# Kernel optimization log

Hardware: AMD Instinct MI355X
Metric: run time of the kernel (lower is better)

The kernel has to match this reference:

```python
import jax, jax.numpy as jnp
import numpy as np

EMBED = 2048
HEADS = 16
GROUPS = 4
HEAD_DIM = EMBED // HEADS  # 128
REPEATS = HEADS // GROUPS  # 4


def setup_inputs() -> dict:
    key = jax.random.key(0)
    ks = jax.random.split(key, 9)
    s = 1.0 / np.sqrt(EMBED)
    kv_dim = GROUPS * HEAD_DIM
    return {
        "x": jax.random.normal(ks[0], (2, 2048, EMBED), dtype=jnp.float32),
        "Wq": jax.random.normal(ks[1], (EMBED, EMBED), dtype=jnp.float32) * s,
        "bq": jnp.zeros((EMBED,), dtype=jnp.float32),
        "Wk": jax.random.normal(ks[2], (EMBED, kv_dim), dtype=jnp.float32) * s,
        "bk": jnp.zeros((kv_dim,), dtype=jnp.float32),
        "Wv": jax.random.normal(ks[3], (EMBED, kv_dim), dtype=jnp.float32) * s,
        "bv": jnp.zeros((kv_dim,), dtype=jnp.float32),
        "Wo": jax.random.normal(ks[4], (EMBED, EMBED), dtype=jnp.float32) * s,
        "bo": jnp.zeros((EMBED,), dtype=jnp.float32),
    }


def reference(x, Wq, bq, Wk, bk, Wv, bv, Wo, bo):
    b, t, e = x.shape
    q = x @ Wq + bq                                   # [b,t,e]
    k = x @ Wk + bk                                   # [b,t,g*d]
    v = x @ Wv + bv
    # [b, g, r, t, d] for q; [b, g, t, d] for k,v (repeat_interleave == group-major)
    q = q.reshape(b, t, GROUPS, REPEATS, HEAD_DIM).transpose(0, 2, 3, 1, 4)
    k = k.reshape(b, t, GROUPS, HEAD_DIM).transpose(0, 2, 1, 3)
    v = v.reshape(b, t, GROUPS, HEAD_DIM).transpose(0, 2, 1, 3)
    scale = 1.0 / np.sqrt(HEAD_DIM)
    scores = jnp.einsum('bgrqd,bgkd->bgrqk', q, k) * scale
    causal = jnp.tril(jnp.ones((t, t), dtype=bool))
    scores = jnp.where(causal, scores, -jnp.inf)
    w = jax.nn.softmax(scores, axis=-1)
    out = jnp.einsum('bgrqk,bgkd->bgrqd', w, v)       # [b,g,r,t,d]
    out = out.transpose(0, 3, 1, 2, 4).reshape(b, t, e)
    return out @ Wo + bo
```

## Files before the change

### kernel.cpp

```cpp
#include <hip/hip_runtime.h>
#include <cstdint>

typedef __bf16 bf16;
typedef __attribute__((ext_vector_type(8))) __bf16 bf16x8;
typedef __attribute__((ext_vector_type(4))) __bf16 bf16x4;
typedef __attribute__((ext_vector_type(4))) float f32x4;

__device__ __forceinline__ void load_lds16(const void* g, void* l) {
  __builtin_amdgcn_global_load_lds(
      (const __attribute__((address_space(1))) unsigned int*)g,
      (__attribute__((address_space(3))) unsigned int*)l, 16, 0, 0);
}

__device__ __forceinline__ float fast_exp2(float x) {
  float r;
  asm volatile("v_exp_f32 %0, %1" : "=v"(r) : "v"(x));
  return r;
}

template <bool OUT_F32>
__global__ __launch_bounds__(256) void gemm_bt(
    const bf16* __restrict__ A, const bf16* __restrict__ Bt,
    const float* __restrict__ bias, void* __restrict__ Cv,
    int M, int N, int K) {
  __shared__ __align__(16) bf16 sA[128 * 64];
  __shared__ __align__(16) bf16 sB[128 * 64];
  const int t = threadIdx.x;
  const int w = t >> 6, lane = t & 63;
  const int quad = lane >> 4, l16 = lane & 15;
  const int wm = (w >> 1) * 64, wn = (w & 1) * 64;
  const int bm = blockIdx.y * 128, bn = blockIdx.x * 128;

  f32x4 acc[4][4] = {};
  const int srow = lane >> 3;
  const int sg = lane & 7;

  for (int kt = 0; kt < (K >> 6); ++kt) {
    const int k0 = kt << 6;
#pragma unroll
    for (int c2 = 0; c2 < 4; ++c2) {
      int c = c2 * 4 + w;
      int row = c * 8 + srow;
      int gg = sg ^ (row & 7);
      load_lds16(A + (int64_t)(bm + row) * K + k0 + gg * 8, sA + c * 512);
      load_lds16(Bt + (int64_t)(bn + row) * K + k0 + gg * 8, sB + c * 512);
    }
    asm volatile("s_waitcnt vmcnt(0)" ::: "memory");
    __syncthreads();
#pragma unroll
    for (int ks = 0; ks < 2; ++ks) {
      bf16x8 af[4], bfr[4];
#pragma unroll
      for (int i = 0; i < 4; ++i) {
        int m = wm + i * 16 + l16;
        af[i] = *(const bf16x8*)(sA + m * 64 + (((ks * 4 + quad) ^ (l16 & 7)) * 8));
        int n = wn + i * 16 + l16;
        bfr[i] = *(const bf16x8*)(sB + n * 64 + (((ks * 4 + quad) ^ (l16 & 7)) * 8));
      }
#pragma unroll
      for (int i = 0; i < 4; ++i)
#pragma unroll
        for (int j = 0; j < 4; ++j)
          acc[i][j] = __builtin_amdgcn_mfma_f32_16x16x32_bf16(af[i], bfr[j],
                                                              acc[i][j], 0, 0, 0);
    }
    __syncthreads();
  }
#pragma unroll
  for (int i = 0; i < 4; ++i) {
    int gm = bm + wm + i * 16 + quad * 4;
#pragma unroll
    for (int j = 0; j < 4; ++j) {
      int gn = bn + wn + j * 16 + l16;
      float bvv = bias ? bias[gn] : 0.0f;
#pragma unroll
      for (int r = 0; r < 4; ++r) {
        float v = acc[i][j][r] + bvv;
        if (OUT_F32)
          ((float*)Cv)[(int64_t)(gm + r) * N + gn] = v;
        else
          ((bf16*)Cv)[(int64_t)(gm + r) * N + gn] = (bf16)v;
      }
    }
  }
}

__global__ __launch_bounds__(256, 2) void attn(
    const bf16* __restrict__ QKV, const bf16* __restrict__ Vt,
    bf16* __restrict__ Out) {
  constexpr float CC = 0.08838834764831845f * 1.44269504088896f;
  __shared__ __align__(16) bf16 sK[2][64 * 128];
  __shared__ __align__(16) bf16 sV[2][128 * 64];
  __shared__ __align__(16) bf16 sP[128 * 64];

  const int t = threadIdx.x;
  const int w = t >> 6, lane = t & 63;
  const int quad = lane >> 4, l16 = lane & 15;
  const int p = blockIdx.x, h = blockIdx.y, b = blockIdx.z;
  const int g = h >> 2;
  const int wr0 = w * 16;
  const int kbase = 2048 + g * 128;
  const bf16* vtb = Vt + (int64_t)((b * 4 + g) * 128) * 2048;
  const int rk = lane >> 4, rv = lane >> 3, sgv = lane & 7;
  const int qrow0A = p * 64, qrow0B = (31 - p) * 64;
  const int niters = 32 - p;

  bf16x8 qreg[2][4];
#pragma unroll
  for (int u = 0; u < 2; ++u) {
    int qr = (u == 0 ? qrow0A : qrow0B);
#pragma unroll
    for (int ks = 0; ks < 4; ++ks)
      qreg[u][ks] = *(const bf16x8*)(QKV +
          (int64_t)(b * 2048 + qr + wr0 + l16) * 3072 + h * 128 + ks * 32 +
          quad * 8);
  }

  f32x4 oacc[2][8] = {};
  float mrow[2] = {-3.0e38f, -3.0e38f};
  float lrow[2] = {0.f, 0.f};

  auto stage = [&](int n0, bf16* sKb, bf16* sVb) {
#pragma unroll
    for (int c2 = 0; c2 < 4; ++c2) {
      int c = c2 * 4 + w;
      int rowk = c * 4 + rk;
      int ggk = (l16 & 8) | ((l16 ^ rowk) & 7);
      load_lds16(QKV + (int64_t)(b * 2048 + n0 + rowk) * 3072 + kbase + ggk * 8,
                 sKb + c * 512);
      int rowv = c * 8 + rv;
      int ggv = sgv ^ (rowv & 7);
      load_lds16(vtb + (int64_t)rowv * 2048 + n0 + ggv * 8, sVb + c * 512);
    }
  };

  stage(0, sK[0], sV[0]);

  const int prowA = wr0 + l16;
  const int prowB = 64 + wr0 + l16;

  for (int it = 0; it < niters; ++it) {
    const int cur = it & 1;
    const int n0 = it * 64;
    bf16* sKc = sK[cur];
    bf16* sVc = sV[cur];
    const bool actA = (it <= p);

    asm volatile("s_waitcnt vmcnt(0)\n\ts_barrier" ::: "memory");
    if (it + 1 < niters) stage(n0 + 64, sK[cur ^ 1], sV[cur ^ 1]);

    f32x4 sacc[2][4] = {};
    if (actA) {
#pragma unroll
      for (int ks = 0; ks < 4; ++ks) {
        bf16x8 ak[4];
#pragma unroll
        for (int mj = 0; mj < 4; ++mj) {
          int kvr = mj * 16 + l16;
          int G = ks * 4 + quad;
          int slot = (G & 8) | ((G ^ kvr) & 7);
          ak[mj] = *(const bf16x8*)(sKc + kvr * 128 + slot * 8);
        }
#pragma unroll
        for (int mj = 0; mj < 4; ++mj) {
          sacc[0][mj] = __builtin_amdgcn_mfma_f32_16x16x32_bf16(
              ak[mj], qreg[0][ks], sacc[0][mj], 0, 0, 0);
          sacc[1][mj] = __builtin_amdgcn_mfma_f32_16x16x32_bf16(
              ak[mj], qreg[1][ks], sacc[1][mj], 0, 0, 0);
        }
      }
    } else {
#pragma unroll
      for (int ks = 0; ks < 4; ++ks) {
        bf16x8 ak[4];
#pragma unroll
        for (int mj = 0; mj < 4; ++mj) {
          int kvr = mj * 16 + l16;
          int G = ks * 4 + quad;
          int slot = (G & 8) | ((G ^ kvr) & 7);
          ak[mj] = *(const bf16x8*)(sKc + kvr * 128 + slot * 8);
        }
#pragma unroll
        for (int mj = 0; mj < 4; ++mj)
          sacc[1][mj] = __builtin_amdgcn_mfma_f32_16x16x32_bf16(
              ak[mj], qreg[1][ks], sacc[1][mj], 0, 0, 0);
      }
    }

    auto softmax_u = [&](int u, bool last, int qrow0u, int prow) {
      if (last) {
        int q = qrow0u + wr0 + l16;
#pragma unroll
        for (int mj = 0; mj < 4; ++mj)
#pragma unroll
          for (int r = 0; r < 4; ++r) {
            int kv = n0 + mj * 16 + quad * 4 + r;
            if (kv > q) sacc[u][mj][r] = -3.0e38f;
          }
      }
      f32x4 m01, m23;
#pragma unroll
      for (int r = 0; r < 4; ++r) {
        m01[r] = fmaxf(sacc[u][0][r], sacc[u][1][r]);
        m23[r] = fmaxf(sacc[u][2][r], sacc[u][3][r]);
      }
      float mx = fmaxf(fmaxf(fmaxf(m01[0], m01[1]), fmaxf(m01[2], m01[3])),
                       fmaxf(fmaxf(m23[0], m23[1]), fmaxf(m23[2], m23[3])));
      mx = fmaxf(mx, __shfl_xor(mx, 16));
      mx = fmaxf(mx, __shfl_xor(mx, 32));
      float mnew = fmaxf(mrow[u], mx);
      float alpha = fast_exp2((mrow[u] - mnew) * CC);
      float rs = 0.f;
#pragma unroll
      for (int mj = 0; mj < 4; ++mj) {
        bf16x4 p4;
#pragma unroll
        for (int r = 0; r < 4; ++r) {
          float pv = fast_exp2((sacc[u][mj][r] - mnew) * CC);
          rs += pv;
          p4[r] = (bf16)pv;
        }
        int g16 = mj * 2 + (quad >> 1);
        int off = prow * 64 + ((g16 ^ (prow & 7)) * 8) + (quad & 1) * 4;
        *(bf16x4*)(sP + off) = p4;
      }
      rs += __shfl_xor(rs, 16);
      rs += __shfl_xor(rs, 32);
      lrow[u] = lrow[u] * alpha + rs;
      mrow[u] = mnew;
#pragma unroll
      for (int dj = 0; dj < 8; ++dj)
#pragma unroll
        for (int r = 0; r < 4; ++r) oacc[u][dj][r] *= alpha;
    };
    if (actA) softmax_u(0, it == p, qrow0A, prowA);
    softmax_u(1, it == niters - 1, qrow0B, prowB);

    asm volatile("s_waitcnt lgkmcnt(0)" ::: "memory");

#pragma unroll
    for (int ks2 = 0; ks2 < 2; ++ks2) {
      int G = ks2 * 4 + quad;
      bf16x8 bpA, bpB;
      if (actA)
        bpA = *(const bf16x8*)(sP + prowA * 64 + ((G ^ (prowA & 7)) * 8));
      bpB = *(const bf16x8*)(sP + prowB * 64 + ((G ^ (prowB & 7)) * 8));
      bf16x8 av[8];
#pragma unroll
      for (int dj = 0; dj < 8; ++dj) {
        int d = dj * 16 + l16;
        av[dj] = *(const bf16x8*)(sVc + d * 64 + ((G ^ (d & 7)) * 8));
      }
      if (actA) {
#pragma unroll
        for (int dj = 0; dj < 8; ++dj) {
          oacc[0][dj] = __builtin_amdgcn_mfma_f32_16x16x32_bf16(
              av[dj], bpA, oacc[0][dj], 0, 0, 0);
          oacc[1][dj] = __builtin_amdgcn_mfma_f32_16x16x32_bf16(
              av[dj], bpB, oacc[1][dj], 0, 0, 0);
        }
      } else {
#pragma unroll
        for (int dj = 0; dj < 8; ++dj)
          oacc[1][dj] = __builtin_amdgcn_mfma_f32_16x16x32_bf16(
              av[dj], bpB, oacc[1][dj], 0, 0, 0);
      }
    }
  }

#pragma unroll
  for (int u = 0; u < 2; ++u) {
    int qrow0u = (u == 0 ? qrow0A : qrow0B);
    float inv = 1.0f / lrow[u];
    int64_t grow = b * 2048 + qrow0u + wr0 + l16;
#pragma unroll
    for (int dj = 0; dj < 8; ++dj) {
      bf16x4 o4;
#pragma unroll
      for (int r = 0; r < 4; ++r) o4[r] = (bf16)(oacc[u][dj][r] * inv);
      *(bf16x4*)(Out + grow * 2048 + h * 128 + dj * 16 + quad * 4) = o4;
    }
  }
}

__global__ void convert_x(const float* __restrict__ x, bf16* __restrict__ xb) {
  int idx = blockIdx.x * 256 + threadIdx.x;
  float4 v = ((const float4*)x)[idx];
  bf16x4 o = {(bf16)v.x, (bf16)v.y, (bf16)v.z, (bf16)v.w};
  ((bf16x4*)xb)[idx] = o;
}

__global__ void transpose_w(const float* __restrict__ W, bf16* __restrict__ Wt,
                            int K, int N) {
  __shared__ float tile[32][33];
  int bx = blockIdx.x, by = blockIdx.y;
  int tx = threadIdx.x, ty = threadIdx.y;
#pragma unroll
  for (int q2 = 0; q2 < 4; ++q2)
    tile[ty + q2 * 8][tx] = W[(int64_t)(by * 32 + ty + q2 * 8) * N + bx * 32 + tx];
  __syncthreads();
#pragma unroll
  for (int q2 = 0; q2 < 4; ++q2)
    Wt[(int64_t)(bx * 32 + ty + q2 * 8) * K + by * 32 + tx] =
        (bf16)tile[tx][ty + q2 * 8];
}

__global__ void transpose_v(const bf16* __restrict__ QKV, bf16* __restrict__ Vt) {
  __shared__ bf16 tile[32][34];
  int dt = blockIdx.x, tt = blockIdx.y, bg = blockIdx.z;
  int b = bg >> 2, g = bg & 3;
  int tx = threadIdx.x, ty = threadIdx.y;
#pragma unroll
  for (int q2 = 0; q2 < 4; ++q2) {
    int trow = tt * 32 + ty + q2 * 8;
    tile[ty + q2 * 8][tx] =
        QKV[(int64_t)(b * 2048 + trow) * 3072 + 2560 + g * 128 + dt * 32 + tx];
  }
  __syncthreads();
#pragma unroll
  for (int q2 = 0; q2 < 4; ++q2) {
    int d = dt * 32 + ty + q2 * 8;
    Vt[(int64_t)(bg * 128 + d) * 2048 + tt * 32 + tx] = tile[tx][ty + q2 * 8];
  }
}

__global__ void concat_bias(const float* __restrict__ bq,
                            const float* __restrict__ bk,
                            const float* __restrict__ bv,
                            float* __restrict__ o) {
  int i = blockIdx.x * 256 + threadIdx.x;
  if (i < 3072)
    o[i] = i < 2048 ? bq[i] : (i < 2560 ? bk[i - 2048] : bv[i - 2560]);
}

extern "C" void kernel_launch(void* const* d_in, const int* in_sizes, int n_in,
                              void* d_out, int out_size, void* d_ws,
                              size_t ws_size, hipStream_t stream) {
  const float* x = (const float*)d_in[0];
  const float* Wq = (const float*)d_in[1];
  const float* bq = (const float*)d_in[2];
  const float* Wk = (const float*)d_in[3];
  const float* bk = (const float*)d_in[4];
  const float* Wv = (const float*)d_in[5];
  const float* bv = (const float*)d_in[6];
  const float* Wo = (const float*)d_in[7];
  const float* bo = (const float*)d_in[8];
  float* out = (float*)d_out;

  char* ws = (char*)d_ws;
  bf16* xb = (bf16*)(ws);
  bf16* wqkvT = (bf16*)(ws + 16777216);
  bf16* woT = (bf16*)(ws + 29360128);
  float* bqkv = (float*)(ws + 37748736);
  bf16* qkv = (bf16*)(ws + 37761024);
  bf16* vt = (bf16*)(ws + 62926848);
  bf16* attnb = (bf16*)(ws + 67121152);

  convert_x<<<8192, 256, 0, stream>>>(x, xb);
  dim3 tb(32, 8);
  transpose_w<<<dim3(64, 64), tb, 0, stream>>>(Wq, wqkvT, 2048, 2048);
  transpose_w<<<dim3(16, 64), tb, 0, stream>>>(Wk, wqkvT + 2048 * 2048, 2048, 512);
  transpose_w<<<dim3(16, 64), tb, 0, stream>>>(Wv, wqkvT + 2560 * 2048, 2048, 512);
  transpose_w<<<dim3(64, 64), tb, 0, stream>>>(Wo, woT, 2048, 2048);
  concat_bias<<<12, 256, 0, stream>>>(bq, bk, bv, bqkv);

  gemm_bt<false><<<dim3(24, 32), 256, 0, stream>>>(xb, wqkvT, bqkv, qkv, 4096,
                                                   3072, 2048);
  transpose_v<<<dim3(4, 64, 8), tb, 0, stream>>>(qkv, vt);
  attn<<<dim3(16, 16, 2), 256, 0, stream>>>(qkv, vt, attnb);
  gemm_bt<true><<<dim3(16, 32), 256, 0, stream>>>(attnb, woT, bo, out, 4096,
                                                  2048, 2048);
}
```

Baseline: 319.1 us.

## Split attention KV range across two blocks with combine kernel, smaller KV tiles

Attention work per query-pair block is split along the KV dimension into two halves (z index), doubling the grid, with each half writing unnormalized outputs plus row max/sum to workspace. A new combine kernel then merges the two partial softmax results. KV tiles shrink from 64 to 32 rows to cut LDS use, and occupancy is raised to 3 blocks per CU. The weight-transpose kernel also moves to 64x64 tiles. The aim is better load balance and occupancy in attention, at the cost of an extra kernel, extra global traffic for the partial outputs, and reuse of workspace regions.

Result: slower. 368.5 us (+15.5%).

```diff
diff --git a/kernel.cpp b/kernel.cpp
--- a/kernel.cpp
+++ b/kernel.cpp
@@ -85,25 +85,32 @@
   }
 }
 
-__global__ __launch_bounds__(256, 2) void attn(
+__global__ __launch_bounds__(256, 3) void attn(
     const bf16* __restrict__ QKV, const bf16* __restrict__ Vt,
-    bf16* __restrict__ Out) {
+    bf16* __restrict__ O1, bf16* __restrict__ O2,
+    float* __restrict__ m_arr, float* __restrict__ l_arr) {
   constexpr float CC = 0.08838834764831845f * 1.44269504088896f;
-  __shared__ __align__(16) bf16 sK[2][64 * 128];
-  __shared__ __align__(16) bf16 sV[2][128 * 64];
-  __shared__ __align__(16) bf16 sP[128 * 64];
+  __shared__ __align__(16) bf16 sK[2][32 * 128];
+  __shared__ __align__(16) bf16 sV[2][128 * 32];
+  __shared__ __align__(16) bf16 sP[128 * 32];
 
   const int t = threadIdx.x;
   const int w = t >> 6, lane = t & 63;
   const int quad = lane >> 4, l16 = lane & 15;
-  const int p = blockIdx.x, h = blockIdx.y, b = blockIdx.z;
+  const int p = blockIdx.x, h = blockIdx.y;
+  const int b = blockIdx.z >> 1, z = blockIdx.z & 1;
   const int g = h >> 2;
   const int wr0 = w * 16;
   const int kbase = 2048 + g * 128;
   const bf16* vtb = Vt + (int64_t)((b * 4 + g) * 128) * 2048;
-  const int rk = lane >> 4, rv = lane >> 3, sgv = lane & 7;
   const int qrow0A = p * 64, qrow0B = (31 - p) * 64;
-  const int niters = 32 - p;
+  const int NV = (z == 0) ? (32 - p) : 33;
+
+  auto map = [&](int vi, int& tl, bool& aA, bool& aB) {
+    if (z == 0) { tl = vi; aA = (vi <= p); aB = true; }
+    else if (vi <= p) { tl = p + 1 + vi; aA = true; aB = false; }
+    else { tl = 31 - 2 * p + vi; aA = false; aB = true; }
+  };
 
   bf16x8 qreg[2][4];
 #pragma unroll
@@ -120,99 +127,93 @@
   float mrow[2] = {-3.0e38f, -3.0e38f};
   float lrow[2] = {0.f, 0.f};
 
-  auto stage = [&](int n0, bf16* sKb, bf16* sVb) {
-#pragma unroll
-    for (int c2 = 0; c2 < 4; ++c2) {
-      int c = c2 * 4 + w;
+  const int rk = lane >> 4;
+  const int rv = lane >> 2, gv = lane & 3;
+
+  auto stage = [&](int tl, int buf) {
+    int n0 = tl * 32;
+#pragma unroll
+    for (int r = 0; r < 2; ++r) {
+      int c = r * 4 + w;
       int rowk = c * 4 + rk;
       int ggk = (l16 & 8) | ((l16 ^ rowk) & 7);
       load_lds16(QKV + (int64_t)(b * 2048 + n0 + rowk) * 3072 + kbase + ggk * 8,
-                 sKb + c * 512);
-      int rowv = c * 8 + rv;
-      int ggv = sgv ^ (rowv & 7);
-      load_lds16(vtb + (int64_t)rowv * 2048 + n0 + ggv * 8, sVb + c * 512);
+                 sK[buf] + c * 512);
+      int rowv = c * 16 + rv;
+      int ggv = gv ^ (rowv & 3);
+      load_lds16(vtb + (int64_t)rowv * 2048 + n0 + ggv * 8, sV[buf] + c * 512);
     }
   };
 
-  stage(0, sK[0], sV[0]);
+  {
+    int tl0; bool a0, b0;
+    map(0, tl0, a0, b0);
+    stage(tl0, 0);
+  }
 
   const int prowA = wr0 + l16;
   const int prowB = 64 + wr0 + l16;
 
-  for (int it = 0; it < niters; ++it) {
-    const int cur = it & 1;
-    const int n0 = it * 64;
+  for (int vi = 0; vi < NV; ++vi) {
+    const int cur = vi & 1;
+    int tl; bool actA, actB;
+    map(vi, tl, actA, actB);
+    const int n0 = tl * 32;
     bf16* sKc = sK[cur];
     bf16* sVc = sV[cur];
-    const bool actA = (it <= p);
 
     asm volatile("s_waitcnt vmcnt(0)\n\ts_barrier" ::: "memory");
-    if (it + 1 < niters) stage(n0 + 64, sK[cur ^ 1], sV[cur ^ 1]);
-
-    f32x4 sacc[2][4] = {};
-    if (actA) {
-#pragma unroll
-      for (int ks = 0; ks < 4; ++ks) {
-        bf16x8 ak[4];
-#pragma unroll
-        for (int mj = 0; mj < 4; ++mj) {
-          int kvr = mj * 16 + l16;
-          int G = ks * 4 + quad;
-          int slot = (G & 8) | ((G ^ kvr) & 7);
-          ak[mj] = *(const bf16x8*)(sKc + kvr * 128 + slot * 8);
-        }
-#pragma unroll
-        for (int mj = 0; mj < 4; ++mj) {
+    if (vi + 1 < NV) {
+      int tln; bool an, bn_;
+      map(vi + 1, tln, an, bn_);
+      stage(tln, cur ^ 1);
+    }
+
+    f32x4 sacc[2][2] = {};
+#pragma unroll
+    for (int ks = 0; ks < 4; ++ks) {
+      bf16x8 ak[2];
+#pragma unroll
+      for (int mj = 0; mj < 2; ++mj) {
+        int kvr = mj * 16 + l16;
+        int G = ks * 4 + quad;
+        int slot = (G & 8) | ((G ^ kvr) & 7);
+        ak[mj] = *(const bf16x8*)(sKc + kvr * 128 + slot * 8);
+      }
+      if (actA)
+#pragma unroll
+        for (int mj = 0; mj < 2; ++mj)
           sacc[0][mj] = __builtin_amdgcn_mfma_f32_16x16x32_bf16(
               ak[mj], qreg[0][ks], sacc[0][mj], 0, 0, 0);
+      if (actB)
+#pragma unroll
+        for (int mj = 0; mj < 2; ++mj)
           sacc[1][mj] = __builtin_amdgcn_mfma_f32_16x16x32_bf16(
               ak[mj], qreg[1][ks], sacc[1][mj], 0, 0, 0);
-        }
-      }
-    } else {
-#pragma unroll
-      for (int ks = 0; ks < 4; ++ks) {
-        bf16x8 ak[4];
-#pragma unroll
-        for (int mj = 0; mj < 4; ++mj) {
-          int kvr = mj * 16 + l16;
-          int G = ks * 4 + quad;
-          int slot = (G & 8) | ((G ^ kvr) & 7);
-          ak[mj] = *(const bf16x8*)(sKc + kvr * 128 + slot * 8);
-        }
-#pragma unroll
-        for (int mj = 0; mj < 4; ++mj)
-          sacc[1][mj] = __builtin_amdgcn_mfma_f32_16x16x32_bf16(
-              ak[mj], qreg[1][ks], sacc[1][mj], 0, 0, 0);
-      }
-    }
-
-    auto softmax_u = [&](int u, bool last, int qrow0u, int prow) {
-      if (last) {
+    }
+
+    auto softmax_u = [&](int u, int qrow0u, int prow) {
+      if (n0 + 31 > qrow0u + wr0) {
         int q = qrow0u + wr0 + l16;
 #pragma unroll
-        for (int mj = 0; mj < 4; ++mj)
+        for (int mj = 0; mj < 2; ++mj)
 #pragma unroll
           for (int r = 0; r < 4; ++r) {
             int kv = n0 + mj * 16 + quad * 4 + r;
             if (kv > q) sacc[u][mj][r] = -3.0e38f;
           }
       }
-      f32x4 m01, m23;
-#pragma unroll
-      for (int r = 0; r < 4; ++r) {
-        m01[r] = fmaxf(sacc[u][0][r], sacc[u][1][r]);
-        m23[r] = fmaxf(sacc[u][2][r], sacc[u][3][r]);
-      }
-      float mx = fmaxf(fmaxf(fmaxf(m01[0], m01[1]), fmaxf(m01[2], m01[3])),
-                       fmaxf(fmaxf(m23[0], m23[1]), fmaxf(m23[2], m23[3])));
+      f32x4 m01;
+#pragma unroll
+      for (int r = 0; r < 4; ++r) m01[r] = fmaxf(sacc[u][0][r], sacc[u][1][r]);
+      float mx = fmaxf(fmaxf(m01[0], m01[1]), fmaxf(m01[2], m01[3]));
       mx = fmaxf(mx, __shfl_xor(mx, 16));
       mx = fmaxf(mx, __shfl_xor(mx, 32));
       float mnew = fmaxf(mrow[u], mx);
       float alpha = fast_exp2((mrow[u] - mnew) * CC);
       float rs = 0.f;
 #pragma unroll
-      for (int mj = 0; mj < 4; ++mj) {
+      for (int mj = 0; mj < 2; ++mj) {
         bf16x4 p4;
 #pragma unroll
         for (int r = 0; r < 4; ++r) {
@@ -221,7 +222,7 @@
           p4[r] = (bf16)pv;
         }
         int g16 = mj * 2 + (quad >> 1);
-        int off = prow * 64 + ((g16 ^ (prow & 7)) * 8) + (quad & 1) * 4;
+        int off = prow * 32 + ((g16 ^ (prow & 3)) * 8) + (quad & 1) * 4;
         *(bf16x4*)(sP + off) = p4;
       }
       rs += __shfl_xor(rs, 16);
@@ -233,54 +234,73 @@
 #pragma unroll
         for (int r = 0; r < 4; ++r) oacc[u][dj][r] *= alpha;
     };
-    if (actA) softmax_u(0, it == p, qrow0A, prowA);
-    softmax_u(1, it == niters - 1, qrow0B, prowB);
+    if (actA) softmax_u(0, qrow0A, prowA);
+    if (actB) softmax_u(1, qrow0B, prowB);
 
     asm volatile("s_waitcnt lgkmcnt(0)" ::: "memory");
 
-#pragma unroll
-    for (int ks2 = 0; ks2 < 2; ++ks2) {
-      int G = ks2 * 4 + quad;
-      bf16x8 bpA, bpB;
+    bf16x8 bpA, bpB;
+    if (actA) bpA = *(const bf16x8*)(sP + prowA * 32 + ((quad ^ (prowA & 3)) * 8));
+    if (actB) bpB = *(const bf16x8*)(sP + prowB * 32 + ((quad ^ (prowB & 3)) * 8));
+#pragma unroll
+    for (int dj = 0; dj < 8; ++dj) {
+      int d = dj * 16 + l16;
+      bf16x8 av = *(const bf16x8*)(sVc + d * 32 + ((quad ^ (d & 3)) * 8));
       if (actA)
-        bpA = *(const bf16x8*)(sP + prowA * 64 + ((G ^ (prowA & 7)) * 8));
-      bpB = *(const bf16x8*)(sP + prowB * 64 + ((G ^ (prowB & 7)) * 8));
-      bf16x8 av[8];
-#pragma unroll
-      for (int dj = 0; dj < 8; ++dj) {
-        int d = dj * 16 + l16;
-        av[dj] = *(const bf16x8*)(sVc + d * 64 + ((G ^ (d & 7)) * 8));
-      }
-      if (actA) {
-#pragma unroll
-        for (int dj = 0; dj < 8; ++dj) {
-          oacc[0][dj] = __builtin_amdgcn_mfma_f32_16x16x32_bf16(
-              av[dj], bpA, oacc[0][dj], 0, 0, 0);
-          oacc[1][dj] = __builtin_amdgcn_mfma_f32_16x16x32_bf16(
-              av[dj], bpB, oacc[1][dj], 0, 0, 0);
-        }
-      } else {
-#pragma unroll
-        for (int dj = 0; dj < 8; ++dj)
-          oacc[1][dj] = __builtin_amdgcn_mfma_f32_16x16x32_bf16(
-              av[dj], bpB, oacc[1][dj], 0, 0, 0);
-      }
-    }
-  }
-
+        oacc[0][dj] = __builtin_amdgcn_mfma_f32_16x16x32_bf16(av, bpA,
+                                                             oacc[0][dj], 0, 0, 0);
+      if (actB)
+        oacc[1][dj] = __builtin_amdgcn_mfma_f32_16x16x32_bf16(av, bpB,
+                                                             oacc[1][dj], 0, 0, 0);
+    }
+  }
+
+  bf16* OutP = (z == 0) ? O1 : O2;
 #pragma unroll
   for (int u = 0; u < 2; ++u) {
     int qrow0u = (u == 0 ? qrow0A : qrow0B);
-    float inv = 1.0f / lrow[u];
     int64_t grow = b * 2048 + qrow0u + wr0 + l16;
 #pragma unroll
     for (int dj = 0; dj < 8; ++dj) {
       bf16x4 o4;
 #pragma unroll
-      for (int r = 0; r < 4; ++r) o4[r] = (bf16)(oacc[u][dj][r] * inv);
-      *(bf16x4*)(Out + grow * 2048 + h * 128 + dj * 16 + quad * 4) = o4;
-    }
-  }
+      for (int r = 0; r < 4; ++r) o4[r] = (bf16)oacc[u][dj][r];
+      *(bf16x4*)(OutP + grow * 2048 + h * 128 + dj * 16 + quad * 4) = o4;
+    }
+    if (quad == 0) {
+      int mi = ((z * 2 + b) * 16 + h) * 2048 + qrow0u + wr0 + l16;
+      m_arr[mi] = mrow[u];
+      l_arr[mi] = lrow[u];
+    }
+  }
+}
+
+__global__ __launch_bounds__(256) void combine(
+    const bf16* __restrict__ O1, const bf16* __restrict__ O2,
+    const float* __restrict__ m_arr, const float* __restrict__ l_arr,
+    bf16* __restrict__ out) {
+  constexpr float CC = 0.08838834764831845f * 1.44269504088896f;
+  int idx = blockIdx.x * 256 + threadIdx.x;
+  int dc = idx & 15;
+  int h = (idx >> 4) & 15;
+  int row = idx >> 8;
+  int b = row >> 11, q = row & 2047;
+  int mi1 = ((0 * 2 + b) * 16 + h) * 2048 + q;
+  int mi2 = ((1 * 2 + b) * 16 + h) * 2048 + q;
+  float m1 = m_arr[mi1], l1 = l_arr[mi1];
+  float m2 = m_arr[mi2], l2 = l_arr[mi2];
+  float mM = fmaxf(m1, m2);
+  float e1 = fast_exp2((m1 - mM) * CC);
+  float e2 = fast_exp2((m2 - mM) * CC);
+  float inv = 1.0f / (e1 * l1 + e2 * l2);
+  int64_t off = (int64_t)row * 2048 + h * 128 + dc * 8;
+  bf16x8 o1 = *(const bf16x8*)(O1 + off);
+  bf16x8 o2 = *(const bf16x8*)(O2 + off);
+  bf16x8 o;
+#pragma unroll
+  for (int e = 0; e < 8; ++e)
+    o[e] = (bf16)(((float)o1[e] * e1 + (float)o2[e] * e2) * inv);
+  *(bf16x8*)(out + off) = o;
 }
 
 __global__ void convert_x(const float* __restrict__ x, bf16* __restrict__ xb) {
@@ -292,17 +312,20 @@
 
 __global__ void transpose_w(const float* __restrict__ W, bf16* __restrict__ Wt,
                             int K, int N) {
-  __shared__ float tile[32][33];
+  __shared__ float tile[64][65];
   int bx = blockIdx.x, by = blockIdx.y;
   int tx = threadIdx.x, ty = threadIdx.y;
 #pragma unroll
-  for (int q2 = 0; q2 < 4; ++q2)
-    tile[ty + q2 * 8][tx] = W[(int64_t)(by * 32 + ty + q2 * 8) * N + bx * 32 + tx];
+  for (int q2 = 0; q2 < 16; ++q2) {
+    int r = ty + q2 * 4;
+    tile[r][tx] = W[(int64_t)(by * 64 + r) * N + bx * 64 + tx];
+  }
   __syncthreads();
 #pragma unroll
-  for (int q2 = 0; q2 < 4; ++q2)
-    Wt[(int64_t)(bx * 32 + ty + q2 * 8) * K + by * 32 + tx] =
-        (bf16)tile[tx][ty + q2 * 8];
+  for (int q2 = 0; q2 < 16; ++q2) {
+    int n = ty + q2 * 4;
+    Wt[(int64_t)(bx * 64 + n) * K + by * 64 + tx] = (bf16)tile[tx][n];
+  }
 }
 
 __global__ void transpose_v(const bf16* __restrict__ QKV, bf16* __restrict__ Vt) {
@@ -354,20 +377,26 @@
   float* bqkv = (float*)(ws + 37748736);
   bf16* qkv = (bf16*)(ws + 37761024);
   bf16* vt = (bf16*)(ws + 62926848);
-  bf16* attnb = (bf16*)(ws + 67121152);
+  bf16* attnO1 = (bf16*)(ws + 67121152);
+  bf16* attnO2 = (bf16*)(ws);
+  float* m_arr = (float*)(ws + 16777216);
+  float* l_arr = (float*)(ws + 16777216 + 524288);
+  bf16* attnb = (bf16*)(ws + 37761024);
 
   convert_x<<<8192, 256, 0, stream>>>(x, xb);
-  dim3 tb(32, 8);
-  transpose_w<<<dim3(64, 64), tb, 0, stream>>>(Wq, wqkvT, 2048, 2048);
-  transpose_w<<<dim3(16, 64), tb, 0, stream>>>(Wk, wqkvT + 2048 * 2048, 2048, 512);
-  transpose_w<<<dim3(16, 64), tb, 0, stream>>>(Wv, wqkvT + 2560 * 2048, 2048, 512);
-  transpose_w<<<dim3(64, 64), tb, 0, stream>>>(Wo, woT, 2048, 2048);
+  dim3 tb(64, 4);
+  transpose_w<<<dim3(32, 32), tb, 0, stream>>>(Wq, wqkvT, 2048, 2048);
+  transpose_w<<<dim3(8, 32), tb, 0, stream>>>(Wk, wqkvT + 2048 * 2048, 2048, 512);
+  transpose_w<<<dim3(8, 32), tb, 0, stream>>>(Wv, wqkvT + 2560 * 2048, 2048, 512);
+  transpose_w<<<dim3(32, 32), tb, 0, stream>>>(Wo, woT, 2048, 2048);
   concat_bias<<<12, 256, 0, stream>>>(bq, bk, bv, bqkv);
 
   gemm_bt<false><<<dim3(24, 32), 256, 0, stream>>>(xb, wqkvT, bqkv, qkv, 4096,
                                                    3072, 2048);
-  transpose_v<<<dim3(4, 64, 8), tb, 0, stream>>>(qkv, vt);
-  attn<<<dim3(16, 16, 2), 256, 0, stream>>>(qkv, vt, attnb);
+  transpose_v<<<dim3(4, 64, 8), dim3(32, 8), 0, stream>>>(qkv, vt);
+  attn<<<dim3(16, 16, 4), 256, 0, stream>>>(qkv, vt, attnO1, attnO2, m_arr,
+                                            l_arr);
+  combine<<<4096, 256, 0, stream>>>(attnO1, attnO2, m_arr, l_arr, attnb);
   gemm_bt<true><<<dim3(16, 32), 256, 0, stream>>>(attnb, woT, bo, out, 4096,
                                                   2048, 2048);
 }
```
